# Kernel tuning notes

Hardware: AMD Instinct MI355X
Metric: run time of the kernel (lower is better)

Reference implementation:

```python
import jax, jax.numpy as jnp
import numpy as np

CH = 512
HEADS = 4
GROUPS = 32  # _groups(512) -> 32
EPS = 1e-5


def setup_inputs() -> dict:
    key = jax.random.key(0)
    ks = jax.random.split(key, 7)
    b, c, h, w = 16, CH, 32, 32
    sd = 1.0 / np.sqrt(c)
    return {
        "x": jax.random.normal(ks[0], (b, c, h, w), dtype=jnp.float32),
        "gamma": jnp.ones((c,), jnp.float32),
        "beta": jnp.zeros((c,), jnp.float32),
        "w_qkv": jax.random.normal(ks[1], (3 * c, c), dtype=jnp.float32) * sd,
        "b_qkv": jax.random.normal(ks[2], (3 * c,), dtype=jnp.float32) * 0.01,
        "w_proj": jax.random.normal(ks[3], (c, c), dtype=jnp.float32) * sd,
        "b_proj": jax.random.normal(ks[4], (c,), dtype=jnp.float32) * 0.01,
    }


def _group_norm(x, gamma, beta):
    b, c, h, w = x.shape
    xg = x.reshape(b, GROUPS, -1)  # (b, G, c//G * h * w)
    mu = jnp.mean(xg, axis=-1, keepdims=True)
    var = jnp.var(xg, axis=-1, keepdims=True)
    xn = ((xg - mu) * jax.lax.rsqrt(var + EPS)).reshape(b, c, h, w)
    return xn * gamma[None, :, None, None] + beta[None, :, None, None]


def reference(x, gamma, beta, w_qkv, b_qkv, w_proj, b_proj):
    b, c, h, w = x.shape
    hd = c // HEADS
    xn = _group_norm(x, gamma, beta)
    # 1x1 conv == channel matmul
    qkv = jnp.einsum('oc,bchw->bohw', w_qkv, xn) + b_qkv[None, :, None, None]
    qkv = qkv.reshape(b, 3, HEADS, hd, h * w)
    q, k, v = qkv[:, 0], qkv[:, 1], qkv[:, 2]  # (b, H, hd, n)
    scale = hd ** -0.5
    attn = jax.nn.softmax(jnp.einsum('bhcn,bhcm->bhnm', q * scale, k), axis=-1)
    out = jnp.einsum('bhnm,bhcm->bhcn', attn, v).reshape(b, c, h, w)
    out = jnp.einsum('oc,bchw->bohw', w_proj, out) + b_proj[None, :, None, None]
    return x + out
```

## Files before the change

### kernel.cpp

```cpp
#include <hip/hip_runtime.h>

#define CH 512
#define HEADS 4
#define HD 128
#define NPIX 1024
#define BATCH 16
#define GROUPS 32
#define GSZ 16
#define EPS 1e-5f

typedef _Float16 f16;
typedef _Float16 f16x8 __attribute__((ext_vector_type(8)));
typedef _Float16 f16x4 __attribute__((ext_vector_type(4)));
typedef float f32x4 __attribute__((ext_vector_type(4)));

__device__ __forceinline__ void gld16(const f16* g, f16* l) {
    __builtin_amdgcn_global_load_lds((__attribute__((address_space(1))) const void*)g,
                                     (__attribute__((address_space(3))) void*)l, 16, 0, 0);
}

__global__ __launch_bounds__(256, 2) void k_pre(const float* __restrict__ x, const float* __restrict__ gamma,
                                                const float* __restrict__ beta, f16* __restrict__ xnT,
                                                const float* __restrict__ wq, const float* __restrict__ wp,
                                                f16* __restrict__ wqT, f16* __restrict__ wpT) {
    __shared__ float xs[GSZ * NPIX];
    __shared__ float red[8];
    __shared__ float stat2[2];
    int bidx = blockIdx.x;
    if (bidx >= 512) {
        int c = (bidx - 512) * 256 + threadIdx.x;
        {
            int ot = c >> 13, kbl = (c >> 7) & 63, ol = c & 127;
            const float* s = wq + ((size_t)(ot * 128 + ol)) * CH + kbl * 8;
            f32x4 a = *(const f32x4*)s, b2 = *(const f32x4*)(s + 4);
            f16x8 v;
            v[0] = (f16)a.x; v[1] = (f16)a.y; v[2] = (f16)a.z; v[3] = (f16)a.w;
            v[4] = (f16)b2.x; v[5] = (f16)b2.y; v[6] = (f16)b2.z; v[7] = (f16)b2.w;
            *(f16x8*)(wqT + (size_t)c * 8) = v;
        }
        if (c < 32768) {
            int ot = c >> 13, kbl = (c >> 7) & 63, ol = c & 127;
            const float* s = wp + ((size_t)(ot * 128 + ol)) * CH + kbl * 8;
            f32x4 a = *(const f32x4*)s, b2 = *(const f32x4*)(s + 4);
            f16x8 v;
            v[0] = (f16)a.x; v[1] = (f16)a.y; v[2] = (f16)a.z; v[3] = (f16)a.w;
            v[4] = (f16)b2.x; v[5] = (f16)b2.y; v[6] = (f16)b2.z; v[7] = (f16)b2.w;
            *(f16x8*)(wpT + (size_t)c * 8) = v;
        }
        return;
    }
    int g = bidx & 31, b = bidx >> 5;
    const f32x4* x4 = (const f32x4*)(x + ((size_t)(b * GROUPS + g)) * (GSZ * NPIX));
    float s = 0.f, ss = 0.f;
    for (int i = threadIdx.x; i < GSZ * NPIX / 4; i += 256) {
        f32x4 v = x4[i];
        *(f32x4*)&xs[i * 4] = v;
        s  += v.x + v.y + v.z + v.w;
        ss += v.x * v.x + v.y * v.y + v.z * v.z + v.w * v.w;
    }
    for (int off = 32; off; off >>= 1) { s += __shfl_down(s, off); ss += __shfl_down(ss, off); }
    int wv = threadIdx.x >> 6, ln = threadIdx.x & 63;
    if (ln == 0) { red[wv] = s; red[4 + wv] = ss; }
    __syncthreads();
    if (threadIdx.x == 0) {
        float S = red[0] + red[1] + red[2] + red[3];
        float SS = red[4] + red[5] + red[6] + red[7];
        float mu = S / (GSZ * NPIX);
        float var = SS / (GSZ * NPIX) - mu * mu;
        stat2[0] = mu; stat2[1] = rsqrtf(var + EPS);
    }
    __syncthreads();
    float mu = stat2[0], rstd = stat2[1];
    int ch = threadIdx.x >> 7;
    int n  = threadIdx.x & 127;
    float gl[8], bl[8];
#pragma unroll
    for (int i = 0; i < 8; i++) {
        float gv = gamma[g * 16 + ch * 8 + i] * rstd;
        gl[i] = gv;
        bl[i] = beta[g * 16 + ch * 8 + i] - mu * gv;
    }
    f16* tb0 = xnT + ((size_t)(b * 8)) * 65536 + (g * 2 + ch) * 1024 + n * 8;
#pragma unroll
    for (int nt = 0; nt < 8; nt++) {
        f16x8 o;
#pragma unroll
        for (int i = 0; i < 8; i++)
            o[i] = (f16)(xs[(ch * 8 + i) * 1024 + nt * 128 + n] * gl[i] + bl[i]);
        *(f16x8*)(tb0 + (size_t)nt * 65536) = o;
    }
}

__global__ __launch_bounds__(256, 3) void k_qkv(const f16* __restrict__ wT, const float* __restrict__ bias,
                                                const f16* __restrict__ xnT, f16* __restrict__ qF,
                                                f16* __restrict__ kTl, f16* __restrict__ vTl) {
    int nt = blockIdx.x, ot = blockIdx.y, b = blockIdx.z;
    int o0 = ot * 128;
    __shared__ union SM {
        struct { f16 As[8192]; f16 Bs[8192]; } s;
        f16 Cf[16384];
    } sm;
    __shared__ float biasS[128];
    if (threadIdx.x < 128) biasS[threadIdx.x] = bias[o0 + threadIdx.x];
    int tid = threadIdx.x, lane = tid & 63, wv = tid >> 6;
    int wr = wv >> 1, wc = wv & 1;
    int l15 = lane & 15, quad = lane >> 4;
    const f16* wA = wT + (size_t)ot * 65536;
    const f16* xB = xnT + ((size_t)(b * 8 + nt)) * 65536;
    f32x4 acc[4][4] = {};
    for (int kk = 0; kk < CH; kk += 64) {
        __syncthreads();
        const f16* sa = wA + (size_t)(kk >> 3) * 1024;
        const f16* sb = xB + (size_t)(kk >> 3) * 1024;
#pragma unroll
        for (int i = 0; i < 4; i++) {
            int s = wv * 4 + i;
            gld16(sa + (size_t)(s * 64 + lane) * 8, sm.s.As + s * 512);
            gld16(sb + (size_t)(s * 64 + lane) * 8, sm.s.Bs + s * 512);
        }
        __syncthreads();
#pragma unroll
        for (int dk = 0; dk < 2; dk++) {
            f16x8 af[4], bf[4];
#pragma unroll
            for (int t = 0; t < 4; t++) {
                af[t] = *(const f16x8*)(sm.s.As + (dk * 4 + quad) * 1024 + (wr * 64 + t * 16 + l15) * 8);
                bf[t] = *(const f16x8*)(sm.s.Bs + (dk * 4 + quad) * 1024 + (wc * 64 + t * 16 + l15) * 8);
            }
#pragma unroll
            for (int tm = 0; tm < 4; tm++)
#pragma unroll
                for (int tn = 0; tn < 4; tn++)
                    acc[tm][tn] = __builtin_amdgcn_mfma_f32_16x16x32_f16(af[tm], bf[tn], acc[tm][tn], 0, 0, 0);
        }
    }
    __syncthreads();
    int which = ot >> 2, h = ot & 3;
#pragma unroll
    for (int tm = 0; tm < 4; tm++)
#pragma unroll
        for (int tn = 0; tn < 4; tn++) {
            int ob = wr * 64 + tm * 16 + quad * 4;
            int n  = wc * 64 + tn * 16 + l15;
            f16x4 pv;
#pragma unroll
            for (int r = 0; r < 4; r++) pv[r] = (f16)(acc[tm][tn][r] + biasS[ob + r]);
            if (which == 0) {
                int addr = ((((n >> 5) * 2 + ((n >> 4) & 1)) * 4 + (ob >> 5)) * 512)
                         + ((ob >> 3) & 3) * 128 + (n & 15) * 8 + (quad & 1) * 4;
                *(f16x4*)&sm.Cf[addr] = pv;
            } else if (which == 1) {
                int addr = (ob >> 3) * 1024 + n * 8 + (quad & 1) * 4;
                *(f16x4*)&sm.Cf[addr] = pv;
            } else {
#pragma unroll
                for (int r = 0; r < 4; r++)
                    sm.Cf[(n >> 3) * 1024 + (ob + r) * 8 + (n & 7)] = pv[r];
            }
        }
    __syncthreads();
    f16* tb = (which == 0) ? (qF + ((size_t)((b * 4 + h) * 8 + nt)) * 16384)
            : (which == 1) ? (kTl + ((size_t)((b * 4 + h) * 8 + nt)) * 16384)
                           : (vTl + ((size_t)((b * 4 + h) * 8 + nt)) * 16384);
#pragma unroll
    for (int i = 0; i < 8; i++) {
        int cid = tid + i * 256;
        *(f16x8*)(tb + (size_t)cid * 8) = *(const f16x8*)(sm.Cf + cid * 8);
    }
}

__global__ __launch_bounds__(512, 4) void k_attn(const f16* __restrict__ qF, const f16* __restrict__ kTl,
                                                 const f16* __restrict__ vTl, f16* __restrict__ oT) {
    __shared__ f16 smem[24576];
    f16* Kl = smem;
    f16* Vl = smem + 8192;
    int bid = blockIdx.x;
    int nt = bid >> 6, group = bid & 63;
    int b = group >> 2, h = group & 3;
    int tid = threadIdx.x, lane = tid & 63, wv = tid >> 6;
    int wq = wv & 3, role = wv >> 2;
    int l15 = lane & 15, quad = lane >> 4;
    const f16* qb = qF + ((size_t)(group * 8 + nt)) * 16384;
    const f16* kb = kTl + (size_t)group * 8 * 16384;
    const f16* vb = vTl + (size_t)group * 8 * 16384;
    f16* Preg = smem + 16384 + wv * 1024;
    f16* dstL = role ? Vl : Kl;

    f16x8 aq[4];
#pragma unroll
    for (int dk = 0; dk < 4; dk++) {
        f16x8 v = *(const f16x8*)(qb + (wv * 4 + dk) * 512 + lane * 8);
        aq[dk] = v * (f16)0.08838834764831845f;
    }

    float m_i = -1e30f, l_i = 0.f;
    f32x4 oaccT[8] = {};

    f16x8 buf[4];
    if (role == 0) {
#pragma unroll
        for (int i = 0; i < 4; i++)
            buf[i] = *(const f16x8*)(kb + (size_t)(wq * 4 + i) * 1024 + lane * 8);
    } else {
#pragma unroll
        for (int i = 0; i < 4; i++)
            buf[i] = *(const f16x8*)(vb + (size_t)(wq * 4 + i) * 512 + lane * 8);
    }

    for (int mc = 0; mc < 16; mc++) {
        __syncthreads();
#pragma unroll
        for (int i = 0; i < 4; i++)
            *(f16x8*)&dstL[(wq * 4 + i) * 512 + lane * 8] = buf[i];
        __syncthreads();

        f32x4 st[4] = {};
#pragma unroll
        for (int dk = 0; dk < 4; dk++) {
            f16x8 kf[4];
#pragma unroll
            for (int t = 0; t < 4; t++)
                kf[t] = *(const f16x8*)&Kl[(dk * 4 + quad) * 512 + (t * 16 + l15) * 8];
#pragma unroll
            for (int tc = 0; tc < 4; tc++)
                st[tc] = __builtin_amdgcn_mfma_f32_16x16x32_f16(kf[tc], aq[dk], st[tc], 0, 0, 0);
        }

        float a[4];
#pragma unroll
        for (int tc = 0; tc < 4; tc++)
            a[tc] = fmaxf(fmaxf(st[tc][0], st[tc][1]), fmaxf(st[tc][2], st[tc][3]));
        a[0] = fmaxf(a[0], a[2]); a[1] = fmaxf(a[1], a[3]);
        float mx = fmaxf(a[0], a[1]);
        mx = fmaxf(mx, __shfl_xor(mx, 16));
        mx = fmaxf(mx, __shfl_xor(mx, 32));
        float mnew = fmaxf(m_i, mx);
        float alpha = __expf(m_i - mnew);
        m_i = mnew;
        float r4[4];
#pragma unroll
        for (int tc = 0; tc < 4; tc++) {
            float p0 = __expf(st[tc][0] - mnew);
            float p1 = __expf(st[tc][1] - mnew);
            float p2 = __expf(st[tc][2] - mnew);
            float p3 = __expf(st[tc][3] - mnew);
            st[tc][0] = p0; st[tc][1] = p1;
            st[tc][2] = p2; st[tc][3] = p3;
            r4[tc] = (p0 + p1) + (p2 + p3);
        }
        float rs = (r4[0] + r4[1]) + (r4[2] + r4[3]);
        rs += __shfl_xor(rs, 16);
        rs += __shfl_xor(rs, 32);
        l_i = l_i * alpha + rs;
#pragma unroll
        for (int tc = 0; tc < 8; tc++) {
            oaccT[tc].x *= alpha; oaccT[tc].y *= alpha;
            oaccT[tc].z *= alpha; oaccT[tc].w *= alpha;
        }

#pragma unroll
        for (int tc = 0; tc < 4; tc++) {
            int blk = tc * 2 + (quad >> 1);
            f16x4 pv;
#pragma unroll
            for (int r = 0; r < 4; r++) pv[r] = (f16)st[tc][r];
            *(f16x4*)&Preg[l15 * 64 + ((blk ^ (l15 & 7)) << 3) + ((quad & 1) << 2)] = pv;
        }

        if (mc < 15) {
            if (role == 0) {
                const f16* s = kb + (size_t)((mc + 1) >> 1) * 16384 + (size_t)((mc + 1) & 1) * 512;
#pragma unroll
                for (int i = 0; i < 4; i++)
                    buf[i] = *(const f16x8*)(s + (size_t)(wq * 4 + i) * 1024 + lane * 8);
            } else {
                const f16* s = vb + (size_t)(mc + 1) * 8192;
#pragma unroll
                for (int i = 0; i < 4; i++)
                    buf[i] = *(const f16x8*)(s + (size_t)(wq * 4 + i) * 512 + lane * 8);
            }
        }

#pragma unroll
        for (int mk = 0; mk < 2; mk++) {
            f16x8 vf[8];
#pragma unroll
            for (int t = 0; t < 8; t++)
                vf[t] = *(const f16x8*)&Vl[(mk * 4 + quad) * 1024 + (t * 16 + l15) * 8];
            int blk = mk * 4 + quad;
            f16x8 pf = *(const f16x8*)&Preg[l15 * 64 + ((blk ^ (l15 & 7)) << 3)];
#pragma unroll
            for (int tc = 0; tc < 8; tc++)
                oaccT[tc] = __builtin_amdgcn_mfma_f32_16x16x32_f16(vf[tc], pf, oaccT[tc], 0, 0, 0);
        }
    }

    __syncthreads();
    {
        float inv = 1.f / l_i;
        int n = wv * 16 + l15;
#pragma unroll
        for (int tc = 0; tc < 8; tc++) {
            int blk = tc * 2 + (quad >> 1);
            f16x4 ov;
#pragma unroll
            for (int r = 0; r < 4; r++) ov[r] = (f16)(oaccT[tc][r] * inv);
            *(f16x4*)&smem[n * 128 + ((blk ^ (n & 15)) << 3) + ((quad & 1) << 2)] = ov;
        }
    }
    __syncthreads();
    f16* ob = oT + ((size_t)(b * 8 + nt)) * 65536;
#pragma unroll
    for (int i = 0; i < 4; i++) {
        int cid = tid + i * 512;
        int cbl = cid >> 7, n = cid & 127;
        f16x8 v = *(const f16x8*)&smem[n * 128 + ((cbl ^ (n & 15)) << 3)];
        *(f16x8*)(ob + (size_t)(h * 16 + cbl) * 1024 + n * 8) = v;
    }
}

__global__ __launch_bounds__(256, 3) void k_proj(const f16* __restrict__ wT, const float* __restrict__ bias,
                                                 const f16* __restrict__ oT, const float* __restrict__ x,
                                                 float* __restrict__ out) {
    int nt = blockIdx.x, ot = blockIdx.y, b = blockIdx.z;
    int n0 = nt * 128, o0 = ot * 128;
    __shared__ union SM {
        struct { f16 As[8192]; f16 Bs[8192]; } s;
        f16 Cs[128][136];
    } sm;
    __shared__ float biasS[128];
    if (threadIdx.x < 128) biasS[threadIdx.x] = bias[o0 + threadIdx.x];
    int tid = threadIdx.x, lane = tid & 63, wv = tid >> 6;
    int wr = wv >> 1, wc = wv & 1;
    int l15 = lane & 15, quad = lane >> 4;
    const f16* wA = wT + (size_t)ot * 65536;
    const f16* xB = oT + ((size_t)(b * 8 + nt)) * 65536;
    f32x4 acc[4][4] = {};
    for (int kk = 0; kk < CH; kk += 64) {
        __syncthreads();
        const f16* sa = wA + (size_t)(kk >> 3) * 1024;
        const f16* sb = xB + (size_t)(kk >> 3) * 1024;
#pragma unroll
        for (int i = 0; i < 4; i++) {
            int s = wv * 4 + i;
            gld16(sa + (size_t)(s * 64 + lane) * 8, sm.s.As + s * 512);
            gld16(sb + (size_t)(s * 64 + lane) * 8, sm.s.Bs + s * 512);
        }
        __syncthreads();
#pragma unroll
        for (int dk = 0; dk < 2; dk++) {
            f16x8 af[4], bf[4];
#pragma unroll
            for (int t = 0; t < 4; t++) {
                af[t] = *(const f16x8*)(sm.s.As + (dk * 4 + quad) * 1024 + (wr * 64 + t * 16 + l15) * 8);
                bf[t] = *(const f16x8*)(sm.s.Bs + (dk * 4 + quad) * 1024 + (wc * 64 + t * 16 + l15) * 8);
            }
#pragma unroll
            for (int tm = 0; tm < 4; tm++)
#pragma unroll
                for (int tn = 0; tn < 4; tn++)
                    acc[tm][tn] = __builtin_amdgcn_mfma_f32_16x16x32_f16(af[tm], bf[tn], acc[tm][tn], 0, 0, 0);
        }
    }
    __syncthreads();
#pragma unroll
    for (int tm = 0; tm < 4; tm++)
#pragma unroll
        for (int tn = 0; tn < 4; tn++)
#pragma unroll
            for (int r = 0; r < 4; r++) {
                int o = wr * 64 + tm * 16 + quad * 4 + r;
                int n = wc * 64 + tn * 16 + l15;
                sm.Cs[o][n] = (f16)(acc[tm][tn][r] + biasS[o]);
            }
    __syncthreads();
#pragma unroll
    for (int i = 0; i < 8; i++) {
        int cid = tid + i * 256;
        int row = cid >> 4, off = (cid & 15) * 8;
        f16x8 v = *(const f16x8*)&sm.Cs[row][off];
        size_t gofs = ((size_t)(b * CH) + o0 + row) * NPIX + n0 + off;
        const float* xp = x + gofs;
        float* op = out + gofs;
        f32x4 o0v, o1v;
        o0v.x = xp[0] + (float)v[0]; o0v.y = xp[1] + (float)v[1];
        o0v.z = xp[2] + (float)v[2]; o0v.w = xp[3] + (float)v[3];
        o1v.x = xp[4] + (float)v[4]; o1v.y = xp[5] + (float)v[5];
        o1v.z = xp[6] + (float)v[6]; o1v.w = xp[7] + (float)v[7];
        *(f32x4*)op = o0v; *(f32x4*)(op + 4) = o1v;
    }
}

extern "C" void kernel_launch(void* const* d_in, const int* in_sizes, int n_in,
                              void* d_out, int out_size, void* d_ws, size_t ws_size,
                              hipStream_t stream) {
    const float* x     = (const float*)d_in[0];
    const float* gamma = (const float*)d_in[1];
    const float* beta  = (const float*)d_in[2];
    const float* wqkv  = (const float*)d_in[3];
    const float* bqkv  = (const float*)d_in[4];
    const float* wproj = (const float*)d_in[5];
    const float* bproj = (const float*)d_in[6];
    float* out = (float*)d_out;

    char* p = (char*)d_ws;
    f16* wqT = (f16*)p;           p += (size_t)3 * CH * CH * 2;
    f16* wpT = (f16*)p;           p += (size_t)CH * CH * 2;
    f16* xnT = (f16*)p;           p += (size_t)BATCH * NPIX * CH * 2;
    f16* qF  = (f16*)p;           p += (size_t)BATCH * HEADS * NPIX * HD * 2;
    f16* kTl = (f16*)p;           p += (size_t)BATCH * HEADS * NPIX * HD * 2;
    f16* vTl = (f16*)p;           p += (size_t)BATCH * HEADS * NPIX * HD * 2;
    f16* oT  = (f16*)p;           p += (size_t)BATCH * NPIX * CH * 2;

    k_pre<<<dim3(896), 256, 0, stream>>>(x, gamma, beta, xnT, wqkv, wproj, wqT, wpT);
    k_qkv<<<dim3(8, 12, BATCH), 256, 0, stream>>>(wqT, bqkv, xnT, qF, kTl, vTl);
    k_attn<<<dim3(512), 512, 0, stream>>>(qF, kTl, vTl, oT);
    k_proj<<<dim3(8, 4, BATCH), 256, 0, stream>>>(wpT, bproj, oT, x, out);
}
```

Before: 196.1 us.

## Keep P in registers via 16x16x16 MFMA, use exp2 and lazy rescaling

The attention kernel no longer round-trips the softmax probabilities through a shared-memory P buffer. It feeds them straight from registers into 16x16x16 MFMAs whose operand layout matches the QK^T accumulator, which also shrinks shared memory. The log2(e) factor is folded into the Q scale so exp2 can be used, and the running-max rescale of the output accumulator is skipped when the wave-wide new max stays within 8 of the old one. The trade-off is twice as many smaller MFMAs and narrower V loads, plus probabilities up to 2^8 held in fp16 before normalization.

```diff
diff --git a/kernel.cpp b/kernel.cpp
--- a/kernel.cpp
+++ b/kernel.cpp
@@ -171,7 +171,7 @@
 
 __global__ __launch_bounds__(512, 4) void k_attn(const f16* __restrict__ qF, const f16* __restrict__ kTl,
                                                  const f16* __restrict__ vTl, f16* __restrict__ oT) {
-    __shared__ f16 smem[24576];
+    __shared__ f16 smem[16384];
     f16* Kl = smem;
     f16* Vl = smem + 8192;
     int bid = blockIdx.x;
@@ -183,14 +183,13 @@
     const f16* qb = qF + ((size_t)(group * 8 + nt)) * 16384;
     const f16* kb = kTl + (size_t)group * 8 * 16384;
     const f16* vb = vTl + (size_t)group * 8 * 16384;
-    f16* Preg = smem + 16384 + wv * 1024;
     f16* dstL = role ? Vl : Kl;
 
     f16x8 aq[4];
 #pragma unroll
     for (int dk = 0; dk < 4; dk++) {
         f16x8 v = *(const f16x8*)(qb + (wv * 4 + dk) * 512 + lane * 8);
-        aq[dk] = v * (f16)0.08838834764831845f;
+        aq[dk] = v * (f16)(0.08838834764831845f * 1.4426950408889634f);
     }
 
     float m_i = -1e30f, l_i = 0.f;
@@ -234,16 +233,22 @@
         float mx = fmaxf(a[0], a[1]);
         mx = fmaxf(mx, __shfl_xor(mx, 16));
         mx = fmaxf(mx, __shfl_xor(mx, 32));
-        float mnew = fmaxf(m_i, mx);
-        float alpha = __expf(m_i - mnew);
-        m_i = mnew;
+
+        bool full = !__all(mx <= m_i + 8.f);
+        float mnew = m_i, alpha = 1.f;
+        if (full) {
+            mnew = fmaxf(m_i, mx);
+            alpha = __builtin_amdgcn_exp2f(m_i - mnew);
+            m_i = mnew;
+        }
+
         float r4[4];
 #pragma unroll
         for (int tc = 0; tc < 4; tc++) {
-            float p0 = __expf(st[tc][0] - mnew);
-            float p1 = __expf(st[tc][1] - mnew);
-            float p2 = __expf(st[tc][2] - mnew);
-            float p3 = __expf(st[tc][3] - mnew);
+            float p0 = __builtin_amdgcn_exp2f(st[tc][0] - mnew);
+            float p1 = __builtin_amdgcn_exp2f(st[tc][1] - mnew);
+            float p2 = __builtin_amdgcn_exp2f(st[tc][2] - mnew);
+            float p3 = __builtin_amdgcn_exp2f(st[tc][3] - mnew);
             st[tc][0] = p0; st[tc][1] = p1;
             st[tc][2] = p2; st[tc][3] = p3;
             r4[tc] = (p0 + p1) + (p2 + p3);
@@ -251,21 +256,22 @@
         float rs = (r4[0] + r4[1]) + (r4[2] + r4[3]);
         rs += __shfl_xor(rs, 16);
         rs += __shfl_xor(rs, 32);
-        l_i = l_i * alpha + rs;
-#pragma unroll
-        for (int tc = 0; tc < 8; tc++) {
-            oaccT[tc].x *= alpha; oaccT[tc].y *= alpha;
-            oaccT[tc].z *= alpha; oaccT[tc].w *= alpha;
-        }
-
-#pragma unroll
-        for (int tc = 0; tc < 4; tc++) {
-            int blk = tc * 2 + (quad >> 1);
-            f16x4 pv;
-#pragma unroll
-            for (int r = 0; r < 4; r++) pv[r] = (f16)st[tc][r];
-            *(f16x4*)&Preg[l15 * 64 + ((blk ^ (l15 & 7)) << 3) + ((quad & 1) << 2)] = pv;
-        }
+        if (full) {
+            l_i = l_i * alpha + rs;
+#pragma unroll
+            for (int tc = 0; tc < 8; tc++) {
+                oaccT[tc].x *= alpha; oaccT[tc].y *= alpha;
+                oaccT[tc].z *= alpha; oaccT[tc].w *= alpha;
+            }
+        } else {
+            l_i += rs;
+        }
+
+        f16x4 pf[4];
+#pragma unroll
+        for (int tc = 0; tc < 4; tc++)
+#pragma unroll
+            for (int r = 0; r < 4; r++) pf[tc][r] = (f16)st[tc][r];
 
         if (mc < 15) {
             if (role == 0) {
@@ -282,16 +288,12 @@
         }
 
 #pragma unroll
-        for (int mk = 0; mk < 2; mk++) {
-            f16x8 vf[8];
-#pragma unroll
-            for (int t = 0; t < 8; t++)
-                vf[t] = *(const f16x8*)&Vl[(mk * 4 + quad) * 1024 + (t * 16 + l15) * 8];
-            int blk = mk * 4 + quad;
-            f16x8 pf = *(const f16x8*)&Preg[l15 * 64 + ((blk ^ (l15 & 7)) << 3)];
-#pragma unroll
-            for (int tc = 0; tc < 8; tc++)
-                oaccT[tc] = __builtin_amdgcn_mfma_f32_16x16x32_f16(vf[tc], pf, oaccT[tc], 0, 0, 0);
+        for (int kblk = 0; kblk < 4; kblk++) {
+#pragma unroll
+            for (int t = 0; t < 8; t++) {
+                f16x4 vf = *(const f16x4*)&Vl[(kblk * 2 + (quad >> 1)) * 1024 + (t * 16 + l15) * 8 + (quad & 1) * 4];
+                oaccT[t] = __builtin_amdgcn_mfma_f32_16x16x16f16(vf, pf[kblk], oaccT[t], 0, 0, 0);
+            }
         }
     }
 
```

New measurement: 221.3 us. +12.8%, slower.
